# Optimization experiments

Hardware: AMD Instinct MI355X
Metric: run time of the kernel (lower is better)

The kernel has to match this reference:

```python
import jax, jax.numpy as jnp
import numpy as np

N_HEADS = 8
D_EMBED = 512
D_CROSS = 768
D_HEAD = D_EMBED // N_HEADS


def setup_inputs() -> dict:
    key = jax.random.key(0)
    ks = jax.random.split(key, 12)
    B, SQ, SKV = 8, 4096, 77
    s_e = 1.0 / np.sqrt(D_EMBED)
    s_c = 1.0 / np.sqrt(D_CROSS)
    return {
        "latent": jax.random.normal(ks[0], (B, SQ, D_EMBED), jnp.float32),
        "context": jax.random.normal(ks[1], (B, SKV, D_CROSS), jnp.float32),
        "wq": jax.random.normal(ks[2], (D_EMBED, D_EMBED), jnp.float32) * s_e,
        "bq": jax.random.normal(ks[3], (D_EMBED,), jnp.float32) * 0.01,
        "wk": jax.random.normal(ks[4], (D_CROSS, D_EMBED), jnp.float32) * s_c,
        "bk": jax.random.normal(ks[5], (D_EMBED,), jnp.float32) * 0.01,
        "wv": jax.random.normal(ks[6], (D_CROSS, D_EMBED), jnp.float32) * s_c,
        "bv": jax.random.normal(ks[7], (D_EMBED,), jnp.float32) * 0.01,
        "wo": jax.random.normal(ks[8], (D_EMBED, D_EMBED), jnp.float32) * s_e,
        "bo": jax.random.normal(ks[9], (D_EMBED,), jnp.float32) * 0.01,
    }


def reference(latent, context, wq, bq, wk, bk, wv, bv, wo, bo):
    B, SQ, _ = latent.shape
    SKV = context.shape[1]
    # projections; weights stored as (in, out)
    q = latent @ wq + bq                     # [B, SQ, D_EMBED]
    k = context @ wk + bk                    # [B, SKV, D_EMBED]
    v = context @ wv + bv                    # [B, SKV, D_EMBED]
    # split heads -> [B, H, S, Dh]
    q = q.reshape(B, SQ, N_HEADS, D_HEAD).transpose(0, 2, 1, 3)
    k = k.reshape(B, SKV, N_HEADS, D_HEAD).transpose(0, 2, 1, 3)
    v = v.reshape(B, SKV, N_HEADS, D_HEAD).transpose(0, 2, 1, 3)
    scale = 1.0 / np.sqrt(D_HEAD).astype(np.float32)
    w = jnp.einsum("bhqd,bhkd->bhqk", q, k) * scale  # [B, H, SQ, SKV]
    w = jax.nn.softmax(w, axis=-1)
    out = jnp.einsum("bhqk,bhkd->bhqd", w, v)        # [B, H, SQ, Dh]
    out = out.transpose(0, 2, 1, 3).reshape(B, SQ, D_EMBED)
    return out @ wo + bo
```

## Files before the change

### kernel.cpp

```cpp
#include <hip/hip_runtime.h>


typedef __attribute__((ext_vector_type(8))) __bf16 bf16x8;
typedef __attribute__((ext_vector_type(4))) float f32x4;

#define DEVI static __device__ __forceinline__

typedef __attribute__((address_space(3))) void lds_void_t;
typedef const __attribute__((address_space(1))) void gbl_void_t;
#define GLDS16(gsrc, ldst) \
  __builtin_amdgcn_global_load_lds((gbl_void_t*)(gsrc), (lds_void_t*)(ldst), 16, 0, 0)

DEVI unsigned short f2bf(float f) {
  unsigned int u = __float_as_uint(f);
  u += 0x7FFFu + ((u >> 16) & 1u);
  return (unsigned short)(u >> 16);
}

DEVI unsigned int pack2bf(float a, float b) {
  return (unsigned int)f2bf(a) | ((unsigned int)f2bf(b) << 16);
}

__global__ __launch_bounds__(256) void cvt_bf16_kernel(const float* __restrict__ in,
                                                       unsigned int* __restrict__ out4) {
  int i = blockIdx.x * 256 + threadIdx.x;
  const float4* in4 = (const float4*)in;
  float4 a = in4[2 * i];
  float4 b = in4[2 * i + 1];
  uint4 o;
  o.x = pack2bf(a.x, a.y);
  o.y = pack2bf(a.z, a.w);
  o.z = pack2bf(b.x, b.y);
  o.w = pack2bf(b.z, b.w);
  *(uint4*)(out4 + 4 * (size_t)i) = o;
}

__global__ __launch_bounds__(256) void wtrans_all_kernel(
    const float* __restrict__ wq, const float* __restrict__ wk,
    const float* __restrict__ wv, const float* __restrict__ wo,
    unsigned short* __restrict__ wqT, unsigned short* __restrict__ wkT,
    unsigned short* __restrict__ wvT, unsigned short* __restrict__ woT) {
  __shared__ float tile[32][33];
  int bid = blockIdx.x;
  const float* in;
  unsigned short* out;
  int K, r;
  if (bid < 256)       { in = wq; out = wqT; K = 512; r = bid; }
  else if (bid < 640)  { in = wk; out = wkT; K = 768; r = bid - 256; }
  else if (bid < 1024) { in = wv; out = wvT; K = 768; r = bid - 640; }
  else                 { in = wo; out = woT; K = 512; r = bid - 1024; }
  int n0 = (r & 15) * 32, k0 = (r >> 4) * 32;
  int tx = threadIdx.x, ty = threadIdx.y;
#pragma unroll
  for (int j = 0; j < 4; ++j)
    tile[ty * 4 + j][tx] = in[(size_t)(k0 + ty * 4 + j) * 512 + n0 + tx];
  __syncthreads();
#pragma unroll
  for (int j = 0; j < 4; ++j)
    out[(size_t)(n0 + ty * 4 + j) * K + k0 + tx] = f2bf(tile[tx][ty * 4 + j]);
}

__global__ __launch_bounds__(256) void kv_proj_kernel(const float* __restrict__ ctx,
                                                      const unsigned short* __restrict__ wkT,
                                                      const unsigned short* __restrict__ wvT,
                                                      const float* __restrict__ bk,
                                                      const float* __restrict__ bv,
                                                      unsigned short* __restrict__ Kp,
                                                      unsigned short* __restrict__ Vt) {
  __shared__ __align__(16) unsigned short As[64][40];
  __shared__ __align__(16) unsigned short Bs[64][40];
  int bid = blockIdx.x;
  int sel = bid / 80;
  int rem = bid % 80;
  int mt = rem / 8, nt = rem % 8;
  const unsigned short* wT = sel ? wvT : wkT;
  const float* bias = sel ? bv : bk;
  int tid = threadIdx.x;
  int l = tid & 63, w = tid >> 6;
  int lr = l & 15, lg = l >> 4;

  f32x4 acc[4] = {};
  for (int k0 = 0; k0 < 768; k0 += 32) {
#pragma unroll
    for (int it = 0; it < 2; ++it) {
      int idx4 = it * 256 + tid;
      int r = idx4 >> 3, q4 = idx4 & 7;
      int m = mt * 64 + r;
      float4 v = {0.f, 0.f, 0.f, 0.f};
      if (m < 616) v = *(const float4*)(ctx + (size_t)m * 768 + k0 + q4 * 4);
      ushort4 o;
      o.x = f2bf(v.x); o.y = f2bf(v.y); o.z = f2bf(v.z); o.w = f2bf(v.w);
      *(ushort4*)&As[r][q4 * 4] = o;
    }
    {
      int c = tid >> 2, q8 = tid & 3;
      *(uint4*)&Bs[c][q8 * 8] =
          *(const uint4*)(wT + (size_t)(nt * 64 + c) * 768 + k0 + q8 * 8);
    }
    __syncthreads();
    bf16x8 a = *(const bf16x8*)&As[w * 16 + lr][lg * 8];
#pragma unroll
    for (int n = 0; n < 4; ++n) {
      bf16x8 bb = *(const bf16x8*)&Bs[n * 16 + lr][lg * 8];
      acc[n] = __builtin_amdgcn_mfma_f32_16x16x32_bf16(a, bb, acc[n], 0, 0, 0);
    }
    __syncthreads();
  }
#pragma unroll
  for (int n = 0; n < 4; ++n) {
#pragma unroll
    for (int reg = 0; reg < 4; ++reg) {
      int m = mt * 64 + w * 16 + lg * 4 + reg;
      if (m < 616) {
        int bI = m / 77, s = m % 77;
        int col = nt * 64 + n * 16 + lr;
        int h = col >> 6, d = col & 63;
        float v = acc[n][reg] + bias[col];
        if (sel == 0)
          Kp[(((size_t)(bI * 8 + h)) * 80 + s) * 64 + d] = f2bf(v);
        else
          Vt[(((size_t)(bI * 8 + h)) * 64 + d) * 96 + s] = f2bf(v);
      }
    }
  }
}

__global__ __launch_bounds__(256, 4) void qproj_attn_kernel(
    const unsigned short* __restrict__ A, const unsigned short* __restrict__ BT,
    const float* __restrict__ bias, const unsigned short* __restrict__ Kp,
    const unsigned short* __restrict__ Vt, unsigned short* __restrict__ Oq) {
  __shared__ __align__(16) char smem[36864];
  unsigned short* As = (unsigned short*)smem;
  unsigned short* Bs = (unsigned short*)(smem + 16384);

  int bid = ((blockIdx.x & 7) << 7) | (blockIdx.x >> 3);
  size_t mbase = (size_t)(bid >> 2) * 128;
  int nbase = (bid & 3) * 128;
  int tid = threadIdx.x;
  int l = tid & 63, w = tid >> 6;
  int lr = l & 15, lg = l >> 4;
  int wr = (w >> 1) * 64, wc = (w & 1) * 64;

  const unsigned short* gA = A + (mbase + w * 32 + (l >> 2)) * 512 + (l & 3) * 8;
  const unsigned short* gB = BT + (size_t)(nbase + w * 32 + (l >> 2)) * 512 + (l & 3) * 8;

  GLDS16(gA, As + w * 1024);
  GLDS16(gA + 16 * 512, As + w * 1024 + 512);
  GLDS16(gB, Bs + w * 1024);
  GLDS16(gB + 16 * 512, Bs + w * 1024 + 512);
  asm volatile("s_waitcnt vmcnt(0)" ::: "memory");
  __syncthreads();

  f32x4 acc[4][4] = {};
#pragma unroll
  for (int k0 = 0; k0 < 512; k0 += 32) {
    const int cur = (k0 >> 5) & 1;
    const int nxt = cur ^ 1;
    if (k0 < 480) {
      GLDS16(gA + k0 + 32, As + nxt * 4096 + w * 1024);
      GLDS16(gA + k0 + 32 + 16 * 512, As + nxt * 4096 + w * 1024 + 512);
      GLDS16(gB + k0 + 32, Bs + nxt * 4096 + w * 1024);
      GLDS16(gB + k0 + 32 + 16 * 512, Bs + nxt * 4096 + w * 1024 + 512);
    }
    const unsigned short* curA = As + cur * 4096;
    const unsigned short* curB = Bs + cur * 4096;
    bf16x8 af[4], bv8[4];
#pragma unroll
    for (int m = 0; m < 4; ++m)
      af[m] = *(const bf16x8*)&curA[(wr + m * 16 + lr) * 32 + lg * 8];
#pragma unroll
    for (int n = 0; n < 4; ++n)
      bv8[n] = *(const bf16x8*)&curB[(wc + n * 16 + lr) * 32 + lg * 8];
#pragma unroll
    for (int m = 0; m < 4; ++m)
#pragma unroll
      for (int n = 0; n < 4; ++n)
        acc[m][n] = __builtin_amdgcn_mfma_f32_16x16x32_bf16(af[m], bv8[n], acc[m][n], 0, 0, 0);
    asm volatile("s_waitcnt vmcnt(0)" ::: "memory");
    __syncthreads();
  }

  unsigned short* Qme = (unsigned short*)smem + w * (64 * 72);
  float bb[4];
#pragma unroll
  for (int n = 0; n < 4; ++n) bb[n] = bias[nbase + wc + n * 16 + lr];
#pragma unroll
  for (int m = 0; m < 4; ++m)
#pragma unroll
    for (int n = 0; n < 4; ++n)
#pragma unroll
      for (int reg = 0; reg < 4; ++reg)
        Qme[(m * 16 + lg * 4 + reg) * 72 + n * 16 + lr] = f2bf(acc[m][n][reg] + bb[n]);

  bf16x8 qf[4][2];
#pragma unroll
  for (int rg = 0; rg < 4; ++rg) {
    qf[rg][0] = *(const bf16x8*)&Qme[(rg * 16 + lr) * 72 + lg * 8];
    qf[rg][1] = *(const bf16x8*)&Qme[(rg * 16 + lr) * 72 + 32 + lg * 8];
  }

  unsigned short* Pme = Qme;
  for (int z = l; z < 256; z += 64) Pme[(z >> 4) * 104 + 80 + (z & 15)] = 0;

  int b = (int)(mbase >> 12);
  int h = (bid & 3) * 2 + (w & 1);
  const unsigned short* Kph = Kp + (size_t)(b * 8 + h) * (80 * 64);
  const unsigned short* Vth = Vt + (size_t)(b * 8 + h) * (64 * 96);

  const float C = 0.125f * 1.44269504088896f;

  auto QK = [&](int rg, f32x4* s) {
#pragma unroll
    for (int t = 0; t < 5; ++t) {
      const unsigned short* kr = Kph + (t * 16 + lr) * 64 + lg * 8;
      bf16x8 k0 = *(const bf16x8*)kr;
      bf16x8 k1 = *(const bf16x8*)(kr + 32);
      s[t] = __builtin_amdgcn_mfma_f32_16x16x32_bf16(qf[rg][0], k0, s[t], 0, 0, 0);
      s[t] = __builtin_amdgcn_mfma_f32_16x16x32_bf16(qf[rg][1], k1, s[t], 0, 0, 0);
    }
    if (lr >= 13) {
      s[4][0] = -1e30f; s[4][1] = -1e30f; s[4][2] = -1e30f; s[4][3] = -1e30f;
    }
  };

  f32x4 sc[5] = {};
  QK(0, sc);
#pragma unroll
  for (int rg = 0; rg < 4; ++rg) {
    float mx[4];
#pragma unroll
    for (int r = 0; r < 4; ++r)
      mx[r] = fmaxf(fmaxf(fmaxf(sc[0][r], sc[1][r]), fmaxf(sc[2][r], sc[3][r])), sc[4][r]);
#pragma unroll
    for (int d = 1; d < 16; d <<= 1)
#pragma unroll
      for (int r = 0; r < 4; ++r) mx[r] = fmaxf(mx[r], __shfl_xor(mx[r], d, 64));
    float p[5][4];
#pragma unroll
    for (int t = 0; t < 5; ++t)
#pragma unroll
      for (int r = 0; r < 4; ++r) p[t][r] = exp2f((sc[t][r] - mx[r]) * C);
#pragma unroll
    for (int t = 0; t < 5; ++t)
#pragma unroll
      for (int r = 0; r < 4; ++r)
        Pme[(lg * 4 + r) * 104 + t * 16 + lr] = f2bf(p[t][r]);

    float sm[4];
#pragma unroll
    for (int r = 0; r < 4; ++r)
      sm[r] = p[0][r] + p[1][r] + p[2][r] + p[3][r] + p[4][r];
#pragma unroll
    for (int d = 1; d < 16; d <<= 1)
#pragma unroll
      for (int r = 0; r < 4; ++r) sm[r] += __shfl_xor(sm[r], d, 64);
    float rs[4];
#pragma unroll
    for (int r = 0; r < 4; ++r) rs[r] = 1.0f / sm[r];

    f32x4 sn[5] = {};
    if (rg < 3) QK(rg + 1, sn);

    bf16x8 ap[3];
#pragma unroll
    for (int c = 0; c < 3; ++c) ap[c] = *(const bf16x8*)&Pme[lr * 104 + c * 32 + lg * 8];
#pragma unroll
    for (int ct = 0; ct < 4; ++ct) {
      f32x4 o = {};
#pragma unroll
      for (int c = 0; c < 3; ++c) {
        bf16x8 vv = *(const bf16x8*)(Vth + (size_t)(ct * 16 + lr) * 96 + c * 32 + lg * 8);
        o = __builtin_amdgcn_mfma_f32_16x16x32_bf16(ap[c], vv, o, 0, 0, 0);
      }
#pragma unroll
      for (int reg = 0; reg < 4; ++reg)
        Oq[(mbase + wr + rg * 16 + lg * 4 + reg) * 512 + nbase + wc + ct * 16 + lr] =
            f2bf(o[reg] * rs[reg]);
    }
#pragma unroll
    for (int t = 0; t < 5; ++t) sc[t] = sn[t];
  }
}

__global__ __launch_bounds__(256) void gemm512_glds_kernel(
    const unsigned short* __restrict__ A, const unsigned short* __restrict__ BT,
    const float* __restrict__ bias, float* __restrict__ Out) {
  __shared__ __align__(16) unsigned short As[2][128 * 32];
  __shared__ __align__(16) unsigned short Bs[2][128 * 32];
  int bid = ((blockIdx.x & 7) << 7) | (blockIdx.x >> 3);
  size_t mbase = (size_t)(bid >> 2) * 128;
  int nbase = (bid & 3) * 128;
  int tid = threadIdx.x;
  int l = tid & 63, w = tid >> 6;
  int lr = l & 15, lg = l >> 4;
  int wr = (w >> 1) * 64, wc = (w & 1) * 64;

  const unsigned short* gA = A + (mbase + w * 32 + (l >> 2)) * 512 + (l & 3) * 8;
  const unsigned short* gB = BT + (size_t)(nbase + w * 32 + (l >> 2)) * 512 + (l & 3) * 8;

  GLDS16(gA, As[0] + w * 1024);
  GLDS16(gA + 16 * 512, As[0] + w * 1024 + 512);
  GLDS16(gB, Bs[0] + w * 1024);
  GLDS16(gB + 16 * 512, Bs[0] + w * 1024 + 512);
  asm volatile("s_waitcnt vmcnt(0)" ::: "memory");
  __syncthreads();

  f32x4 acc[4][4] = {};
#pragma unroll
  for (int k0 = 0; k0 < 512; k0 += 32) {
    const int cur = (k0 >> 5) & 1;
    const int nxt = cur ^ 1;
    if (k0 < 480) {
      GLDS16(gA + k0 + 32, As[nxt] + w * 1024);
      GLDS16(gA + k0 + 32 + 16 * 512, As[nxt] + w * 1024 + 512);
      GLDS16(gB + k0 + 32, Bs[nxt] + w * 1024);
      GLDS16(gB + k0 + 32 + 16 * 512, Bs[nxt] + w * 1024 + 512);
    }
    bf16x8 af[4], bv8[4];
#pragma unroll
    for (int m = 0; m < 4; ++m)
      af[m] = *(const bf16x8*)&As[cur][(wr + m * 16 + lr) * 32 + lg * 8];
#pragma unroll
    for (int n = 0; n < 4; ++n)
      bv8[n] = *(const bf16x8*)&Bs[cur][(wc + n * 16 + lr) * 32 + lg * 8];
#pragma unroll
    for (int m = 0; m < 4; ++m)
#pragma unroll
      for (int n = 0; n < 4; ++n)
        acc[m][n] = __builtin_amdgcn_mfma_f32_16x16x32_bf16(af[m], bv8[n], acc[m][n], 0, 0, 0);
    asm volatile("s_waitcnt vmcnt(0)" ::: "memory");
    __syncthreads();
  }
#pragma unroll
  for (int m = 0; m < 4; ++m) {
#pragma unroll
    for (int n = 0; n < 4; ++n) {
#pragma unroll
      for (int reg = 0; reg < 4; ++reg) {
        size_t row = mbase + wr + m * 16 + lg * 4 + reg;
        int col = nbase + wc + n * 16 + lr;
        Out[row * 512 + col] = acc[m][n][reg] + bias[col];
      }
    }
  }
}

static const size_t OFF_Q   = 0;
static const size_t OFF_KP  = 33554432;
static const size_t OFF_VT  = OFF_KP + 655360;
static const size_t OFF_WQT = OFF_VT + 786432;
static const size_t OFF_WKT = OFF_WQT + 524288;
static const size_t OFF_WVT = OFF_WKT + 786432;
static const size_t OFF_WOT = OFF_WVT + 786432;
static const size_t WS_NEEDED = OFF_WOT + 524288;

extern "C" void kernel_launch(void* const* d_in, const int* in_sizes, int n_in,
                              void* d_out, int out_size, void* d_ws, size_t ws_size,
                              hipStream_t stream) {
  (void)in_sizes; (void)n_in; (void)out_size;
  if (ws_size < WS_NEEDED) return;

  const float* latent  = (const float*)d_in[0];
  const float* context = (const float*)d_in[1];
  const float* wq = (const float*)d_in[2];
  const float* bq = (const float*)d_in[3];
  const float* wk = (const float*)d_in[4];
  const float* bk = (const float*)d_in[5];
  const float* wv = (const float*)d_in[6];
  const float* bv = (const float*)d_in[7];
  const float* wo = (const float*)d_in[8];
  const float* bo = (const float*)d_in[9];
  float* out = (float*)d_out;

  char* ws = (char*)d_ws;
  unsigned short* wsQ = (unsigned short*)(ws + OFF_Q);
  unsigned short* Kp  = (unsigned short*)(ws + OFF_KP);
  unsigned short* Vt  = (unsigned short*)(ws + OFF_VT);
  unsigned short* wqT = (unsigned short*)(ws + OFF_WQT);
  unsigned short* wkT = (unsigned short*)(ws + OFF_WKT);
  unsigned short* wvT = (unsigned short*)(ws + OFF_WVT);
  unsigned short* woT = (unsigned short*)(ws + OFF_WOT);

  unsigned short* latBF = (unsigned short*)d_out;

  wtrans_all_kernel<<<1280, dim3(32, 8), 0, stream>>>(wq, wk, wv, wo,
                                                      wqT, wkT, wvT, woT);
  hipMemsetAsync(ws + OFF_KP, 0, 655360 + 786432, stream);
  kv_proj_kernel<<<160, 256, 0, stream>>>(context, wkT, wvT, bk, bv, Kp, Vt);
  cvt_bf16_kernel<<<8192, 256, 0, stream>>>(latent, (unsigned int*)latBF);
  qproj_attn_kernel<<<1024, 256, 0, stream>>>(latBF, wqT, bq, Kp, Vt, wsQ);
  gemm512_glds_kernel<<<1024, 256, 0, stream>>>(wsQ, woT, bo, out);
}
```

Before: 127.1 us.

## Give each wave private LDS tiles to drop block barriers in GEMM loops

Each wave now loads its own 64-row A and B slices into a private double-buffered LDS region, so the per-k-step __syncthreads is replaced by per-wave waitcnt ordering and the next tile's loads stay in flight during the MFMAs. This removes block-wide barrier stalls in both the fused Q-projection/attention kernel and the output projection GEMM. The cost is duplicated global-to-LDS traffic, since the two waves sharing rows or columns now each fetch them, plus 64 KB of LDS per block, with launch bounds lowered to 2 blocks per CU.

```diff
diff --git a/kernel.cpp b/kernel.cpp
--- a/kernel.cpp
+++ b/kernel.cpp
@@ -125,13 +125,11 @@
   }
 }
 
-__global__ __launch_bounds__(256, 4) void qproj_attn_kernel(
+__global__ __launch_bounds__(256, 2) void qproj_attn_kernel(
     const unsigned short* __restrict__ A, const unsigned short* __restrict__ BT,
     const float* __restrict__ bias, const unsigned short* __restrict__ Kp,
     const unsigned short* __restrict__ Vt, unsigned short* __restrict__ Oq) {
-  __shared__ __align__(16) char smem[36864];
-  unsigned short* As = (unsigned short*)smem;
-  unsigned short* Bs = (unsigned short*)(smem + 16384);
+  __shared__ __align__(16) unsigned short smem[32768];
 
   int bid = ((blockIdx.x & 7) << 7) | (blockIdx.x >> 3);
   size_t mbase = (size_t)(bid >> 2) * 128;
@@ -141,46 +139,48 @@
   int lr = l & 15, lg = l >> 4;
   int wr = (w >> 1) * 64, wc = (w & 1) * 64;
 
-  const unsigned short* gA = A + (mbase + w * 32 + (l >> 2)) * 512 + (l & 3) * 8;
-  const unsigned short* gB = BT + (size_t)(nbase + w * 32 + (l >> 2)) * 512 + (l & 3) * 8;
-
-  GLDS16(gA, As + w * 1024);
-  GLDS16(gA + 16 * 512, As + w * 1024 + 512);
-  GLDS16(gB, Bs + w * 1024);
-  GLDS16(gB + 16 * 512, Bs + w * 1024 + 512);
-  asm volatile("s_waitcnt vmcnt(0)" ::: "memory");
-  __syncthreads();
+  unsigned short* wbase = smem + w * 8192;
+
+  const unsigned short* gA = A + (mbase + wr + (l >> 2)) * 512 + (l & 3) * 8;
+  const unsigned short* gB = BT + (size_t)(nbase + wc + (l >> 2)) * 512 + (l & 3) * 8;
+
+  auto stage = [&](int k0, int b) {
+#pragma unroll
+    for (int c = 0; c < 4; ++c) {
+      GLDS16(gA + (size_t)(c * 16) * 512 + k0, wbase + b * 4096 + c * 512);
+      GLDS16(gB + (size_t)(c * 16) * 512 + k0, wbase + b * 4096 + 2048 + c * 512);
+    }
+  };
 
   f32x4 acc[4][4] = {};
-#pragma unroll
-  for (int k0 = 0; k0 < 512; k0 += 32) {
-    const int cur = (k0 >> 5) & 1;
-    const int nxt = cur ^ 1;
-    if (k0 < 480) {
-      GLDS16(gA + k0 + 32, As + nxt * 4096 + w * 1024);
-      GLDS16(gA + k0 + 32 + 16 * 512, As + nxt * 4096 + w * 1024 + 512);
-      GLDS16(gB + k0 + 32, Bs + nxt * 4096 + w * 1024);
-      GLDS16(gB + k0 + 32 + 16 * 512, Bs + nxt * 4096 + w * 1024 + 512);
-    }
-    const unsigned short* curA = As + cur * 4096;
-    const unsigned short* curB = Bs + cur * 4096;
+  stage(0, 0);
+#pragma unroll
+  for (int t = 0; t < 16; ++t) {
+    const int cur = t & 1;
+    if (t < 15) {
+      asm volatile("s_waitcnt lgkmcnt(0)" ::: "memory");
+      stage((t + 1) * 32, cur ^ 1);
+      asm volatile("s_waitcnt vmcnt(8)" ::: "memory");
+    } else {
+      asm volatile("s_waitcnt vmcnt(0)" ::: "memory");
+    }
+    const unsigned short* bufA = wbase + cur * 4096;
+    const unsigned short* bufB = bufA + 2048;
     bf16x8 af[4], bv8[4];
 #pragma unroll
     for (int m = 0; m < 4; ++m)
-      af[m] = *(const bf16x8*)&curA[(wr + m * 16 + lr) * 32 + lg * 8];
+      af[m] = *(const bf16x8*)&bufA[(m * 16 + lr) * 32 + lg * 8];
 #pragma unroll
     for (int n = 0; n < 4; ++n)
-      bv8[n] = *(const bf16x8*)&curB[(wc + n * 16 + lr) * 32 + lg * 8];
+      bv8[n] = *(const bf16x8*)&bufB[(n * 16 + lr) * 32 + lg * 8];
 #pragma unroll
     for (int m = 0; m < 4; ++m)
 #pragma unroll
       for (int n = 0; n < 4; ++n)
         acc[m][n] = __builtin_amdgcn_mfma_f32_16x16x32_bf16(af[m], bv8[n], acc[m][n], 0, 0, 0);
-    asm volatile("s_waitcnt vmcnt(0)" ::: "memory");
-    __syncthreads();
-  }
-
-  unsigned short* Qme = (unsigned short*)smem + w * (64 * 72);
+  }
+
+  unsigned short* Qme = wbase;
   float bb[4];
 #pragma unroll
   for (int n = 0; n < 4; ++n) bb[n] = bias[nbase + wc + n * 16 + lr];
@@ -282,11 +282,10 @@
   }
 }
 
-__global__ __launch_bounds__(256) void gemm512_glds_kernel(
+__global__ __launch_bounds__(256, 2) void gemm512_glds_kernel(
     const unsigned short* __restrict__ A, const unsigned short* __restrict__ BT,
     const float* __restrict__ bias, float* __restrict__ Out) {
-  __shared__ __align__(16) unsigned short As[2][128 * 32];
-  __shared__ __align__(16) unsigned short Bs[2][128 * 32];
+  __shared__ __align__(16) unsigned short smem[32768];
   int bid = ((blockIdx.x & 7) << 7) | (blockIdx.x >> 3);
   size_t mbase = (size_t)(bid >> 2) * 128;
   int nbase = (bid & 3) * 128;
@@ -295,41 +294,44 @@
   int lr = l & 15, lg = l >> 4;
   int wr = (w >> 1) * 64, wc = (w & 1) * 64;
 
-  const unsigned short* gA = A + (mbase + w * 32 + (l >> 2)) * 512 + (l & 3) * 8;
-  const unsigned short* gB = BT + (size_t)(nbase + w * 32 + (l >> 2)) * 512 + (l & 3) * 8;
-
-  GLDS16(gA, As[0] + w * 1024);
-  GLDS16(gA + 16 * 512, As[0] + w * 1024 + 512);
-  GLDS16(gB, Bs[0] + w * 1024);
-  GLDS16(gB + 16 * 512, Bs[0] + w * 1024 + 512);
-  asm volatile("s_waitcnt vmcnt(0)" ::: "memory");
-  __syncthreads();
+  unsigned short* wbase = smem + w * 8192;
+  const unsigned short* gA = A + (mbase + wr + (l >> 2)) * 512 + (l & 3) * 8;
+  const unsigned short* gB = BT + (size_t)(nbase + wc + (l >> 2)) * 512 + (l & 3) * 8;
+
+  auto stage = [&](int k0, int b) {
+#pragma unroll
+    for (int c = 0; c < 4; ++c) {
+      GLDS16(gA + (size_t)(c * 16) * 512 + k0, wbase + b * 4096 + c * 512);
+      GLDS16(gB + (size_t)(c * 16) * 512 + k0, wbase + b * 4096 + 2048 + c * 512);
+    }
+  };
 
   f32x4 acc[4][4] = {};
-#pragma unroll
-  for (int k0 = 0; k0 < 512; k0 += 32) {
-    const int cur = (k0 >> 5) & 1;
-    const int nxt = cur ^ 1;
-    if (k0 < 480) {
-      GLDS16(gA + k0 + 32, As[nxt] + w * 1024);
-      GLDS16(gA + k0 + 32 + 16 * 512, As[nxt] + w * 1024 + 512);
-      GLDS16(gB + k0 + 32, Bs[nxt] + w * 1024);
-      GLDS16(gB + k0 + 32 + 16 * 512, Bs[nxt] + w * 1024 + 512);
-    }
+  stage(0, 0);
+#pragma unroll
+  for (int t = 0; t < 16; ++t) {
+    const int cur = t & 1;
+    if (t < 15) {
+      asm volatile("s_waitcnt lgkmcnt(0)" ::: "memory");
+      stage((t + 1) * 32, cur ^ 1);
+      asm volatile("s_waitcnt vmcnt(8)" ::: "memory");
+    } else {
+      asm volatile("s_waitcnt vmcnt(0)" ::: "memory");
+    }
+    const unsigned short* bufA = wbase + cur * 4096;
+    const unsigned short* bufB = bufA + 2048;
     bf16x8 af[4], bv8[4];
 #pragma unroll
     for (int m = 0; m < 4; ++m)
-      af[m] = *(const bf16x8*)&As[cur][(wr + m * 16 + lr) * 32 + lg * 8];
+      af[m] = *(const bf16x8*)&bufA[(m * 16 + lr) * 32 + lg * 8];
 #pragma unroll
     for (int n = 0; n < 4; ++n)
-      bv8[n] = *(const bf16x8*)&Bs[cur][(wc + n * 16 + lr) * 32 + lg * 8];
+      bv8[n] = *(const bf16x8*)&bufB[(n * 16 + lr) * 32 + lg * 8];
 #pragma unroll
     for (int m = 0; m < 4; ++m)
 #pragma unroll
       for (int n = 0; n < 4; ++n)
         acc[m][n] = __builtin_amdgcn_mfma_f32_16x16x32_bf16(af[m], bv8[n], acc[m][n], 0, 0, 0);
-    asm volatile("s_waitcnt vmcnt(0)" ::: "memory");
-    __syncthreads();
   }
 #pragma unroll
   for (int m = 0; m < 4; ++m) {
```

Measured after the change: 137.2 us. 1.08x slower.

## Deepen GEMM K-loop prefetch with split barriers and merge prep kernels

Applied to the files above, without the earlier changes.

Rewrites the K-loops of both the Q-projection/attention kernel and the output GEMM so that two stages are prefetched ahead. Each step waits with a partial vmcnt, reads its fragments into registers, then issues the next global-to-LDS loads into the same buffer before running the MFMAs. This hides more load latency instead of waiting for every load to finish on each step. It also folds the latent fp32-to-bf16 conversion into the weight-transpose kernel, removing one launch. The tradeoff is an extra barrier per step and reliance on correct vmcnt accounting.

```diff
diff --git a/kernel.cpp b/kernel.cpp
--- a/kernel.cpp
+++ b/kernel.cpp
@@ -21,27 +21,28 @@
   return (unsigned int)f2bf(a) | ((unsigned int)f2bf(b) << 16);
 }
 
-__global__ __launch_bounds__(256) void cvt_bf16_kernel(const float* __restrict__ in,
-                                                       unsigned int* __restrict__ out4) {
-  int i = blockIdx.x * 256 + threadIdx.x;
-  const float4* in4 = (const float4*)in;
-  float4 a = in4[2 * i];
-  float4 b = in4[2 * i + 1];
-  uint4 o;
-  o.x = pack2bf(a.x, a.y);
-  o.y = pack2bf(a.z, a.w);
-  o.z = pack2bf(b.x, b.y);
-  o.w = pack2bf(b.z, b.w);
-  *(uint4*)(out4 + 4 * (size_t)i) = o;
-}
-
-__global__ __launch_bounds__(256) void wtrans_all_kernel(
+__global__ __launch_bounds__(256) void prep_kernel(
     const float* __restrict__ wq, const float* __restrict__ wk,
     const float* __restrict__ wv, const float* __restrict__ wo,
     unsigned short* __restrict__ wqT, unsigned short* __restrict__ wkT,
-    unsigned short* __restrict__ wvT, unsigned short* __restrict__ woT) {
+    unsigned short* __restrict__ wvT, unsigned short* __restrict__ woT,
+    const float* __restrict__ latent, unsigned int* __restrict__ latBF4) {
+  int bid = blockIdx.x;
+  int tid = threadIdx.x;
+  if (bid >= 1280) {
+    size_t i = (size_t)(bid - 1280) * 256 + tid;
+    const float4* in4 = (const float4*)latent;
+    float4 a = in4[2 * i];
+    float4 b = in4[2 * i + 1];
+    uint4 o;
+    o.x = pack2bf(a.x, a.y);
+    o.y = pack2bf(a.z, a.w);
+    o.z = pack2bf(b.x, b.y);
+    o.w = pack2bf(b.z, b.w);
+    *(uint4*)(latBF4 + 4 * i) = o;
+    return;
+  }
   __shared__ float tile[32][33];
-  int bid = blockIdx.x;
   const float* in;
   unsigned short* out;
   int K, r;
@@ -50,7 +51,7 @@
   else if (bid < 1024) { in = wv; out = wvT; K = 768; r = bid - 640; }
   else                 { in = wo; out = woT; K = 512; r = bid - 1024; }
   int n0 = (r & 15) * 32, k0 = (r >> 4) * 32;
-  int tx = threadIdx.x, ty = threadIdx.y;
+  int tx = tid & 31, ty = tid >> 5;
 #pragma unroll
   for (int j = 0; j < 4; ++j)
     tile[ty * 4 + j][tx] = in[(size_t)(k0 + ty * 4 + j) * 512 + n0 + tx];
@@ -125,13 +126,42 @@
   }
 }
 
+#define KSTEP(t, boff)                                                        \
+  {                                                                           \
+    if ((t) < 15)                                                             \
+      asm volatile("s_waitcnt vmcnt(4)" ::: "memory");                        \
+    else                                                                      \
+      asm volatile("s_waitcnt vmcnt(0)" ::: "memory");                        \
+    __builtin_amdgcn_s_barrier();                                             \
+    __builtin_amdgcn_sched_barrier(0);                                        \
+    const unsigned short* bufA = smem + (boff);                               \
+    const unsigned short* bufB = bufA + 4096;                                 \
+    bf16x8 af[4], bv8[4];                                                     \
+    _Pragma("unroll") for (int m = 0; m < 4; ++m)                             \
+        af[m] = *(const bf16x8*)&bufA[(wr + m * 16 + lr) * 32 + lg * 8];      \
+    _Pragma("unroll") for (int n = 0; n < 4; ++n)                             \
+        bv8[n] = *(const bf16x8*)&bufB[(wc + n * 16 + lr) * 32 + lg * 8];     \
+    asm volatile("s_waitcnt lgkmcnt(0)" ::: "memory");                        \
+    __builtin_amdgcn_sched_barrier(0);                                        \
+    __builtin_amdgcn_s_barrier();                                             \
+    if ((t) <= 13) {                                                          \
+      int nk = ((t) + 2) * 32;                                                \
+      GLDS16(gA + nk, smem + (boff) + w * 1024);                              \
+      GLDS16(gA + nk + 16 * 512, smem + (boff) + w * 1024 + 512);             \
+      GLDS16(gB + nk, smem + (boff) + 4096 + w * 1024);                       \
+      GLDS16(gB + nk + 16 * 512, smem + (boff) + 4096 + w * 1024 + 512);      \
+    }                                                                         \
+    _Pragma("unroll") for (int m = 0; m < 4; ++m)                             \
+        _Pragma("unroll") for (int n = 0; n < 4; ++n)                         \
+            acc[m][n] = __builtin_amdgcn_mfma_f32_16x16x32_bf16(              \
+                af[m], bv8[n], acc[m][n], 0, 0, 0);                           \
+  }
+
 __global__ __launch_bounds__(256, 4) void qproj_attn_kernel(
     const unsigned short* __restrict__ A, const unsigned short* __restrict__ BT,
     const float* __restrict__ bias, const unsigned short* __restrict__ Kp,
     const unsigned short* __restrict__ Vt, unsigned short* __restrict__ Oq) {
-  __shared__ __align__(16) char smem[36864];
-  unsigned short* As = (unsigned short*)smem;
-  unsigned short* Bs = (unsigned short*)(smem + 16384);
+  __shared__ __align__(16) unsigned short smem[18432];
 
   int bid = ((blockIdx.x & 7) << 7) | (blockIdx.x >> 3);
   size_t mbase = (size_t)(bid >> 2) * 128;
@@ -144,43 +174,23 @@
   const unsigned short* gA = A + (mbase + w * 32 + (l >> 2)) * 512 + (l & 3) * 8;
   const unsigned short* gB = BT + (size_t)(nbase + w * 32 + (l >> 2)) * 512 + (l & 3) * 8;
 
-  GLDS16(gA, As + w * 1024);
-  GLDS16(gA + 16 * 512, As + w * 1024 + 512);
-  GLDS16(gB, Bs + w * 1024);
-  GLDS16(gB + 16 * 512, Bs + w * 1024 + 512);
-  asm volatile("s_waitcnt vmcnt(0)" ::: "memory");
-  __syncthreads();
+  GLDS16(gA, smem + w * 1024);
+  GLDS16(gA + 16 * 512, smem + w * 1024 + 512);
+  GLDS16(gB, smem + 4096 + w * 1024);
+  GLDS16(gB + 16 * 512, smem + 4096 + w * 1024 + 512);
+  GLDS16(gA + 32, smem + 8192 + w * 1024);
+  GLDS16(gA + 32 + 16 * 512, smem + 8192 + w * 1024 + 512);
+  GLDS16(gB + 32, smem + 12288 + w * 1024);
+  GLDS16(gB + 32 + 16 * 512, smem + 12288 + w * 1024 + 512);
 
   f32x4 acc[4][4] = {};
-#pragma unroll
-  for (int k0 = 0; k0 < 512; k0 += 32) {
-    const int cur = (k0 >> 5) & 1;
-    const int nxt = cur ^ 1;
-    if (k0 < 480) {
-      GLDS16(gA + k0 + 32, As + nxt * 4096 + w * 1024);
-      GLDS16(gA + k0 + 32 + 16 * 512, As + nxt * 4096 + w * 1024 + 512);
-      GLDS16(gB + k0 + 32, Bs + nxt * 4096 + w * 1024);
-      GLDS16(gB + k0 + 32 + 16 * 512, Bs + nxt * 4096 + w * 1024 + 512);
-    }
-    const unsigned short* curA = As + cur * 4096;
-    const unsigned short* curB = Bs + cur * 4096;
-    bf16x8 af[4], bv8[4];
-#pragma unroll
-    for (int m = 0; m < 4; ++m)
-      af[m] = *(const bf16x8*)&curA[(wr + m * 16 + lr) * 32 + lg * 8];
-#pragma unroll
-    for (int n = 0; n < 4; ++n)
-      bv8[n] = *(const bf16x8*)&curB[(wc + n * 16 + lr) * 32 + lg * 8];
-#pragma unroll
-    for (int m = 0; m < 4; ++m)
-#pragma unroll
-      for (int n = 0; n < 4; ++n)
-        acc[m][n] = __builtin_amdgcn_mfma_f32_16x16x32_bf16(af[m], bv8[n], acc[m][n], 0, 0, 0);
-    asm volatile("s_waitcnt vmcnt(0)" ::: "memory");
-    __syncthreads();
-  }
-
-  unsigned short* Qme = (unsigned short*)smem + w * (64 * 72);
+#pragma unroll 1
+  for (int t = 0; t < 16; t += 2) {
+    KSTEP(t, 0);
+    KSTEP(t + 1, 8192);
+  }
+
+  unsigned short* Qme = smem + w * (64 * 72);
   float bb[4];
 #pragma unroll
   for (int n = 0; n < 4; ++n) bb[n] = bias[nbase + wc + n * 16 + lr];
@@ -285,8 +295,7 @@
 __global__ __launch_bounds__(256) void gemm512_glds_kernel(
     const unsigned short* __restrict__ A, const unsigned short* __restrict__ BT,
     const float* __restrict__ bias, float* __restrict__ Out) {
-  __shared__ __align__(16) unsigned short As[2][128 * 32];
-  __shared__ __align__(16) unsigned short Bs[2][128 * 32];
+  __shared__ __align__(16) unsigned short smem[16384];
   int bid = ((blockIdx.x & 7) << 7) | (blockIdx.x >> 3);
   size_t mbase = (size_t)(bid >> 2) * 128;
   int nbase = (bid & 3) * 128;
@@ -298,39 +307,22 @@
   const unsigned short* gA = A + (mbase + w * 32 + (l >> 2)) * 512 + (l & 3) * 8;
   const unsigned short* gB = BT + (size_t)(nbase + w * 32 + (l >> 2)) * 512 + (l & 3) * 8;
 
-  GLDS16(gA, As[0] + w * 1024);
-  GLDS16(gA + 16 * 512, As[0] + w * 1024 + 512);
-  GLDS16(gB, Bs[0] + w * 1024);
-  GLDS16(gB + 16 * 512, Bs[0] + w * 1024 + 512);
-  asm volatile("s_waitcnt vmcnt(0)" ::: "memory");
-  __syncthreads();
+  GLDS16(gA, smem + w * 1024);
+  GLDS16(gA + 16 * 512, smem + w * 1024 + 512);
+  GLDS16(gB, smem + 4096 + w * 1024);
+  GLDS16(gB + 16 * 512, smem + 4096 + w * 1024 + 512);
+  GLDS16(gA + 32, smem + 8192 + w * 1024);
+  GLDS16(gA + 32 + 16 * 512, smem + 8192 + w * 1024 + 512);
+  GLDS16(gB + 32, smem + 12288 + w * 1024);
+  GLDS16(gB + 32 + 16 * 512, smem + 12288 + w * 1024 + 512);
 
   f32x4 acc[4][4] = {};
-#pragma unroll
-  for (int k0 = 0; k0 < 512; k0 += 32) {
-    const int cur = (k0 >> 5) & 1;
-    const int nxt = cur ^ 1;
-    if (k0 < 480) {
-      GLDS16(gA + k0 + 32, As[nxt] + w * 1024);
-      GLDS16(gA + k0 + 32 + 16 * 512, As[nxt] + w * 1024 + 512);
-      GLDS16(gB + k0 + 32, Bs[nxt] + w * 1024);
-      GLDS16(gB + k0 + 32 + 16 * 512, Bs[nxt] + w * 1024 + 512);
-    }
-    bf16x8 af[4], bv8[4];
-#pragma unroll
-    for (int m = 0; m < 4; ++m)
-      af[m] = *(const bf16x8*)&As[cur][(wr + m * 16 + lr) * 32 + lg * 8];
-#pragma unroll
-    for (int n = 0; n < 4; ++n)
-      bv8[n] = *(const bf16x8*)&Bs[cur][(wc + n * 16 + lr) * 32 + lg * 8];
-#pragma unroll
-    for (int m = 0; m < 4; ++m)
-#pragma unroll
-      for (int n = 0; n < 4; ++n)
-        acc[m][n] = __builtin_amdgcn_mfma_f32_16x16x32_bf16(af[m], bv8[n], acc[m][n], 0, 0, 0);
-    asm volatile("s_waitcnt vmcnt(0)" ::: "memory");
-    __syncthreads();
-  }
+#pragma unroll 1
+  for (int t = 0; t < 16; t += 2) {
+    KSTEP(t, 0);
+    KSTEP(t + 1, 8192);
+  }
+
 #pragma unroll
   for (int m = 0; m < 4; ++m) {
 #pragma unroll
@@ -383,11 +375,11 @@
 
   unsigned short* latBF = (unsigned short*)d_out;
 
-  wtrans_all_kernel<<<1280, dim3(32, 8), 0, stream>>>(wq, wk, wv, wo,
-                                                      wqT, wkT, wvT, woT);
+  prep_kernel<<<1280 + 8192, 256, 0, stream>>>(wq, wk, wv, wo, wqT, wkT, wvT,
+                                               woT, latent,
+                                               (unsigned int*)latBF);
   hipMemsetAsync(ws + OFF_KP, 0, 655360 + 786432, stream);
   kv_proj_kernel<<<160, 256, 0, stream>>>(context, wkT, wvT, bk, bv, Kp, Vt);
-  cvt_bf16_kernel<<<8192, 256, 0, stream>>>(latent, (unsigned int*)latBF);
   qproj_attn_kernel<<<1024, 256, 0, stream>>>(latBF, wqT, bq, Kp, Vt, wsQ);
   gemm512_glds_kernel<<<1024, 256, 0, stream>>>(wsQ, woT, bo, out);
 }
```

Result: no change. 125.1 us (-1.6%).
